# Optimization experiments

Hardware: AMD Instinct MI355X
Metric: run time of the kernel (lower is better)

## Reference

```python
import jax, jax.numpy as jnp
import numpy as np

B, L, C = 64, 64, 16          # batch, seq_len, chars per word
V, CV = 100000, 100           # word vocab, char vocab
EMB, CHD = 300, 64            # word emb dim, char emb dim
N_HIGHWAY, N_ATTN = 2, 2
D = EMB + 3 * 50              # highway_dim = 450


def setup_inputs() -> dict:
    ks = jax.random.split(jax.random.key(0), 16)
    word_emb = jax.random.normal(ks[6], (V, EMB), jnp.float32) * 0.01
    word_emb = word_emb.at[0].set(0.0)  # padding_idx row zeroed
    return {
        "q1": jax.random.randint(ks[0], (B, L), 0, V),
        "q2": jax.random.randint(ks[1], (B, L), 0, V),
        "q1_len": jax.random.randint(ks[2], (B,), 1, L + 1),
        "q2_len": jax.random.randint(ks[3], (B,), 1, L + 1),
        "q1_char": jax.random.randint(ks[4], (B, L, C), 0, CV),
        "q2_char": jax.random.randint(ks[5], (B, L, C), 0, CV),
        "word_emb": word_emb,
        "char_emb": jax.random.normal(ks[7], (CV, CHD), jnp.float32) * 0.1,
        "conv_w3": jax.random.normal(ks[8], (50, CHD, 3), jnp.float32) / np.sqrt(CHD * 3),
        "conv_b3": jnp.zeros((50,), jnp.float32),
        "conv_w4": jax.random.normal(ks[9], (50, CHD, 4), jnp.float32) / np.sqrt(CHD * 4),
        "conv_b4": jnp.zeros((50,), jnp.float32),
        "conv_w5": jax.random.normal(ks[10], (50, CHD, 5), jnp.float32) / np.sqrt(CHD * 5),
        "conv_b5": jnp.zeros((50,), jnp.float32),
        "hw_w": jax.random.normal(ks[11], (D, D), jnp.float32) / np.sqrt(D),
        "hw_b": jnp.zeros((D,), jnp.float32),
        "attn_w": jax.random.normal(ks[12], (N_ATTN, 3 * D), jnp.float32) / np.sqrt(3 * D),
        "attn_b": jnp.zeros((N_ATTN,), jnp.float32),
    }


def _char_features(qc, emb, convs):
    # qc: [B, T, C] int -> [B, T, 150]
    Bq, T, Cc = qc.shape
    e = emb[qc.reshape(-1, Cc)].transpose(0, 2, 1)  # [B*T, CHD, C]
    outs = []
    for w, b in convs:
        h = jax.lax.conv_general_dilated(e, w, (1,), 'VALID',
                                         dimension_numbers=('NCH', 'OIH', 'NCH'))
        h = jax.nn.relu(h + b[None, :, None])
        outs.append(jnp.max(h, axis=2))  # max over char positions
    return jnp.concatenate(outs, axis=-1).reshape(Bq, T, -1)


def _highway(x, w, b):
    # NB: original reuses the SAME linear for transform and gate (bug-faithful)
    y = x @ w.T + b
    g = jax.nn.sigmoid(y)
    return g * jax.nn.relu(y) + (1.0 - g) * x


def _self_attn(x, mask, w, b):
    # Exact decomposition of Linear(concat(x_i, x_j, x_i*x_j)) -> scalar:
    # score[b,i,j] = x_i.w1 + x_j.w2 + sum_d x_i x_j w3 + b
    d = x.shape[-1]
    w1, w2, w3 = w[:d], w[d:2 * d], w[2 * d:]
    scores = ((x @ w1)[:, :, None] + (x @ w2)[:, None, :]
              + jnp.einsum('bid,bjd->bij', x * w3, x) + b)
    # original masked_fill uses -1e-09 (not -1e9) -- reproduce faithfully
    logits = jnp.where(mask[:, None, :], scores, jnp.float32(-1e-9))
    attn = jax.nn.softmax(logits, axis=-1)
    return jnp.einsum('bij,bjd->bid', attn, x)


def _branch(q, q_char, q_len, word_emb, char_emb, convs, hw_w, hw_b, attn_w, attn_b):
    mask = jnp.arange(L)[None, :] < q_len[:, None]
    x = jnp.concatenate([word_emb[q], _char_features(q_char, char_emb, convs)], axis=-1)
    for _ in range(N_HIGHWAY):
        x = _highway(x, hw_w, hw_b)
    att = x
    for i in range(N_ATTN):
        att = _self_attn(x, mask, attn_w[i], attn_b[i])
        x = att + x
    return att


def reference(q1, q2, q1_len, q2_len, q1_char, q2_char, word_emb, char_emb,
              conv_w3, conv_b3, conv_w4, conv_b4, conv_w5, conv_b5,
              hw_w, hw_b, attn_w, attn_b):
    convs = [(conv_w3, conv_b3), (conv_w4, conv_b4), (conv_w5, conv_b5)]
    a1 = _branch(q1, q1_char, q1_len, word_emb, char_emb, convs, hw_w, hw_b, attn_w, attn_b)
    a2 = _branch(q2, q2_char, q2_len, word_emb, char_emb, convs, hw_w, hw_b, attn_w, attn_b)
    return (a1, a2)
```

## Files before the change

kernel.cpp:

```cpp
#include <hip/hip_runtime.h>
#include <math.h>

#define B   64
#define L   64
#define C   16
#define CHD 64
#define EMB 300
#define D   450
#define DP  480
#define NT  (B*L)
#define NBH 128

typedef short bf16x8 __attribute__((ext_vector_type(8)));
typedef float f32x4  __attribute__((ext_vector_type(4)));
typedef float f32x2  __attribute__((ext_vector_type(2)));
typedef unsigned short ushort_t;
typedef ushort_t us4 __attribute__((ext_vector_type(4)));

#define MFMA16 __builtin_amdgcn_mfma_f32_16x16x32_bf16

#define WPF_N (10 * 10 * 512)
#define WBF_N (32 * 15 * 512)
#define XFRAG 30720

#define XFS 456
#define XSS 488

__device__ inline float wave_sum(float v) {
#pragma unroll
    for (int o = 32; o; o >>= 1) v += __shfl_xor(v, o, 64);
    return v;
}
__device__ inline ushort_t f2b(float f) {
    union { float f; unsigned u; } c; c.f = f;
    unsigned r = c.u + 0x7FFFu + ((c.u >> 16) & 1u);
    return (ushort_t)(r >> 16);
}

__global__ __launch_bounds__(256) void prep_kernel(
    const float* __restrict__ W,
    const float* __restrict__ w3, const float* __restrict__ b3,
    const float* __restrict__ w4, const float* __restrict__ b4,
    const float* __restrict__ w5, const float* __restrict__ b5,
    const float* __restrict__ char_emb,
    ushort_t* __restrict__ Wb16F, ushort_t* __restrict__ WpadF,
    float* __restrict__ bias160, ushort_t* __restrict__ ceb16)
{
    int idx = blockIdx.x * 256 + threadIdx.x;
    if (idx < WBF_N) {
        const int e = idx & 7, l = (idx >> 3) & 63, t = idx >> 9;
        const int ks = t % 15, nt = t / 15;
        const int ln = l & 15, q = l >> 4;
        const int n = nt * 16 + ln, k = ks * 32 + q * 8 + e;
        float v = (n < D && k < D) ? W[(size_t)n * D + k] : 0.f;
        Wb16F[idx] = f2b(v);
        return;
    }
    idx -= WBF_N;
    if (idx < WPF_N) {
        const int e = idx & 7, l = (idx >> 3) & 63, t = idx >> 9;
        const int ks = t % 10, nt = t / 10;
        const int ln = l & 15, q = l >> 4;
        const int f = nt * 16 + ln;
        const int kd = ks * 32 + q * 8 + e;
        const int k = kd >> 6, d = kd & 63;
        float v = 0.f;
        if (f < 50)       { if (k < 3) v = w3[f * 192 + d * 3 + k]; }
        else if (f < 100) { if (k < 4) v = w4[(f - 50) * 256 + d * 4 + k]; }
        else if (f < 150) { v = w5[(f - 100) * 320 + d * 5 + k]; }
        WpadF[idx] = f2b(v);
        return;
    }
    idx -= WPF_N;
    if (idx < 160) {
        bias160[idx] = (idx < 50) ? b3[idx] : (idx < 100) ? b4[idx - 50]
                     : (idx < 150) ? b5[idx - 100] : 0.f;
    } else if (idx < 160 + 100 * 64) {
        int i = idx - 160;
        ceb16[i] = f2b(char_emb[i]);
    }
}

#define ESS 72
#define EST (20 * ESS)

__global__ __launch_bounds__(256) void embed_conv_kernel(
    const int* __restrict__ q1, const int* __restrict__ q2,
    const int* __restrict__ q1c, const int* __restrict__ q2c,
    const float* __restrict__ word_emb, const ushort_t* __restrict__ ceb16,
    const ushort_t* __restrict__ WpadF, const float* __restrict__ bias160,
    float* __restrict__ xout, ushort_t* __restrict__ xbF)
{
    __shared__ ushort_t es[8 * EST];
    __shared__ ushort_t Xt[8 * XSS];

    const int tid  = threadIdx.x;
    const int wv   = tid >> 6;
    const int lane = tid & 63;
    const int ln   = lane & 15, quad = lane >> 4;
    const int bx   = blockIdx.x;
    const int tokbase = ((bx & 7) * 128 + (bx >> 3)) * 8;

#pragma unroll
    for (int i = 0; i < 4; ++i) {
        int c = tid + i * 256;
        int row = c >> 3, part = c & 7;
        int tl = row >> 4, cr = row & 15;
        int gtok   = tokbase + tl;
        int branch = gtok >> 12;
        int tokl   = gtok & (NT - 1);
        int cid    = (branch ? q2c : q1c)[tokl * C + cr];
        *(bf16x8*)&es[tl * EST + cr * ESS + part * 8] =
            *(const bf16x8*)&ceb16[cid * 64 + part * 8];
    }
    {
        int tl = tid >> 5, rr = (tid >> 3) & 3, part = tid & 7;
        bf16x8 z = {0, 0, 0, 0, 0, 0, 0, 0};
        *(bf16x8*)&es[tl * EST + (16 + rr) * ESS + part * 8] = z;
    }

#pragma unroll 1
    for (int c = tid; c < 8 * 75; c += 256) {
        const int t  = c / 75, d4 = c - t * 75;
        const int tok    = tokbase + t;
        const int branch = tok >> 12;
        const int tokl   = tok & (NT - 1);
        const int w      = (branch ? q2 : q1)[tokl];
        const float4 v = *(const float4*)(word_emb + (size_t)w * EMB + d4 * 4);
        float* dst = xout + (size_t)tok * D + d4 * 4;
        *(f32x2*)dst       = (f32x2){v.x, v.y};
        *(f32x2*)(dst + 2) = (f32x2){v.z, v.w};
        us4 pk = { f2b(v.x), f2b(v.y), f2b(v.z), f2b(v.w) };
        *(us4*)&Xt[t * XSS + d4 * 4] = pk;
    }
    if (tid < 240) {
        const int t = tid / 30, k = tid - t * 30;
        Xt[t * XSS + D + k] = 0;
    }
    __syncthreads();

    const int t0 = wv * 2, t1 = t0 + 1;
    f32x4 acc[2][10];
#pragma unroll
    for (int t = 0; t < 2; ++t)
#pragma unroll
        for (int nt = 0; nt < 10; ++nt) acc[t][nt] = (f32x4){0.f, 0.f, 0.f, 0.f};

#pragma unroll 1
    for (int ks = 0; ks < 10; ++ks) {
        const int kk   = ks * 32 + quad * 8;
        const int arow = kk >> 6, aoff = kk & 63;
        bf16x8 a0 = *(const bf16x8*)&es[t0 * EST + (ln + arow) * ESS + aoff];
        bf16x8 a1 = *(const bf16x8*)&es[t1 * EST + (ln + arow) * ESS + aoff];
#pragma unroll
        for (int nt = 0; nt < 10; ++nt) {
            bf16x8 bf = *(const bf16x8*)&WpadF[(size_t)((nt * 10 + ks) << 9) + lane * 8];
            acc[0][nt] = MFMA16(a0, bf, acc[0][nt], 0, 0, 0);
            acc[1][nt] = MFMA16(a1, bf, acc[1][nt], 0, 0, 0);
        }
    }
    __syncthreads();

    float* smf = (float*)es;
#pragma unroll
    for (int t = 0; t < 2; ++t) {
        const int tloc = t0 + t;
#pragma unroll
        for (int nt = 0; nt < 10; ++nt) {
            const int f  = nt * 16 + ln;
            const int Pf = (f < 50) ? 14 : (f < 100) ? 13 : 12;
            float m = -1e30f;
#pragma unroll
            for (int r = 0; r < 4; ++r) {
                const int p = quad * 4 + r;
                if (p < Pf) m = fmaxf(m, acc[t][nt][r]);
            }
            m = fmaxf(m, __shfl_xor(m, 16, 64));
            m = fmaxf(m, __shfl_xor(m, 32, 64));
            if (quad == 0) smf[tloc * 160 + f] = fmaxf(0.f, m + bias160[f]);
        }
    }
    __syncthreads();
#pragma unroll 1
    for (int c = tid; c < 8 * 150; c += 256) {
        const int t = c / 150, f = c - t * 150;
        const float rv = smf[t * 160 + f];
        xout[(size_t)(tokbase + t) * D + EMB + f] = rv;
        Xt[t * XSS + EMB + f] = f2b(rv);
    }
    __syncthreads();

    {
        const int tile = tokbase >> 4, half = (tokbase >> 3) & 1;
#pragma unroll 1
        for (int c = tid; c < 480; c += 256) {
            const int ksl = c >> 5, s = c & 31;
            const int q = s >> 3, tl = s & 7;
            const int l = q * 16 + half * 8 + tl;
            bf16x8 v = *(const bf16x8*)&Xt[tl * XSS + ksl * 32 + q * 8];
            *(bf16x8*)&xbF[((size_t)(tile * 15 + ksl) * 64 + l) * 8] = v;
        }
    }
}

#define HLS 72

__global__ __launch_bounds__(256, 4) void highway_mfma_kernel(
    const ushort_t* __restrict__ xbFi, const float* __restrict__ xf32,
    const ushort_t* __restrict__ Wb16F, const float* __restrict__ bvec,
    float* __restrict__ out, ushort_t* __restrict__ xbFo)
{
    __shared__ ushort_t Xl[64 * HLS];

    const int bx = blockIdx.x;
    const int cx = bx & 7, rr = bx >> 3;
    const int my = cx * 16 + (rr & 15);
    const int mx = rr >> 4;

    const int tid  = threadIdx.x;
    const int wv   = tid >> 6;
    const int lane = tid & 63;
    const int wm = wv >> 1, wn = wv & 1;
    const int m0 = my * 64 + wm * 32;
    const int n0 = mx * 64 + wn * 32;
    const int lm = lane & 15, quad = lane >> 4;

    const int tA0 = my * 4 + wm * 2;
    const ushort_t* ax0 = xbFi + (size_t)(tA0 * 15) * 512 + lane * 8;
    const ushort_t* ax1 = ax0 + 15 * 512;
    const int ntg0 = mx * 4 + wn * 2;
    const ushort_t* bw0 = Wb16F + (size_t)(ntg0 * 15) * 512 + lane * 8;
    const ushort_t* bw1 = bw0 + 15 * 512;

    f32x4 acc[2][2];
#pragma unroll
    for (int i = 0; i < 2; ++i)
#pragma unroll
        for (int j = 0; j < 2; ++j) acc[i][j] = (f32x4){0.f, 0.f, 0.f, 0.f};

#pragma unroll 3
    for (int ks = 0; ks < 15; ++ks) {
        bf16x8 a0 = *(const bf16x8*)(ax0 + ks * 512);
        bf16x8 a1 = *(const bf16x8*)(ax1 + ks * 512);
        bf16x8 b0 = *(const bf16x8*)(bw0 + ks * 512);
        bf16x8 b1 = *(const bf16x8*)(bw1 + ks * 512);
        acc[0][0] = MFMA16(a0, b0, acc[0][0], 0, 0, 0);
        acc[0][1] = MFMA16(a0, b1, acc[0][1], 0, 0, 0);
        acc[1][0] = MFMA16(a1, b0, acc[1][0], 0, 0, 0);
        acc[1][1] = MFMA16(a1, b1, acc[1][1], 0, 0, 0);
    }

#pragma unroll
    for (int nt = 0; nt < 2; ++nt) {
        const int n  = n0 + nt * 16 + lm;
        const int nl = wn * 32 + nt * 16 + lm;
        const bool nval = (n < D);
        const float bv = nval ? bvec[n] : 0.f;
#pragma unroll
        for (int mt = 0; mt < 2; ++mt) {
#pragma unroll
            for (int r = 0; r < 4; ++r) {
                const int m  = m0 + mt * 16 + quad * 4 + r;
                const int ml = wm * 32 + mt * 16 + quad * 4 + r;
                float y = acc[mt][nt][r] + bv;
                float g = 1.f / (1.f + __expf(-y));
                float o = 0.f;
                if (nval) {
                    float xo = xf32[(size_t)m * D + n];
                    o = g * fmaxf(y, 0.f) + (1.f - g) * xo;
                    out[(size_t)m * D + n] = o;
                }
                Xl[ml * HLS + nl] = f2b(nval ? o : 0.f);
            }
        }
    }
    __syncthreads();

#pragma unroll 1
    for (int c = tid; c < 512; c += 256) {
        const int fi = c >> 6, l = c & 63;
        const int tl = fi >> 1, ksl = fi & 1;
        const int ksg = mx * 2 + ksl;
        if (ksg < 15) {
            const int lnp = l & 15, qp = l >> 4;
            bf16x8 v = *(const bf16x8*)&Xl[(tl * 16 + lnp) * HLS + ksl * 32 + qp * 8];
            *(bf16x8*)&xbFo[((size_t)((my * 4 + tl) * 15 + ksg) * 64 + l) * 8] = v;
        }
    }
}

__global__ __launch_bounds__(256) void highway2_prep_kernel(
    const ushort_t* __restrict__ xbFi, const float* __restrict__ xf32in,
    const ushort_t* __restrict__ Wb16F, const float* __restrict__ bvec,
    const float* __restrict__ attn_w,
    float* __restrict__ outf, ushort_t* __restrict__ xbFo,
    ushort_t* __restrict__ xw3F, ushort_t* __restrict__ xTF,
    float* __restrict__ s1g, float* __restrict__ s2g)
{
    __shared__ float    Xf[16 * XFS];
    __shared__ ushort_t Xs[16 * XSS];

    const int bx  = blockIdx.x;
    const int wid = (bx & 7) * 64 + (bx >> 3);
    const int bh  = wid >> 2, jq = wid & 3;
    const int tt  = wid;
    const int m0  = tt * 16;
    const int tid = threadIdx.x;
    const int wv  = tid >> 6;
    const int lane = tid & 63;
    const int ln = lane & 15, quad = lane >> 4;

    if (tid < 480) {
        const int t = tid / 30, k = tid - t * 30;
        Xs[t * XSS + D + k] = 0;
    }

    const ushort_t* ax = xbFi + (size_t)(tt * 15) * 512 + lane * 8;
    f32x4 acc[8];
#pragma unroll
    for (int t = 0; t < 8; ++t) acc[t] = (f32x4){0.f, 0.f, 0.f, 0.f};

#pragma unroll 1
    for (int ks = 0; ks < 15; ++ks) {
        bf16x8 a = *(const bf16x8*)(ax + ks * 512);
#pragma unroll
        for (int t = 0; t < 8; ++t) {
            const int nt = wv * 8 + t;
            if (nt < 30) {
                bf16x8 b = *(const bf16x8*)&Wb16F[(size_t)(nt * 15 + ks) * 512 + lane * 8];
                acc[t] = MFMA16(a, b, acc[t], 0, 0, 0);
            }
        }
    }

#pragma unroll
    for (int t = 0; t < 8; ++t) {
        const int nt = wv * 8 + t;
        if (nt >= 30) continue;
        const int n = nt * 16 + ln;
        const bool nval = (n < D);
        const float bv = nval ? bvec[n] : 0.f;
#pragma unroll
        for (int reg = 0; reg < 4; ++reg) {
            const int i = quad * 4 + reg;
            float y = acc[t][reg] + bv;
            float g = 1.f / (1.f + __expf(-y));
            if (nval) {
                float xo = xf32in[(size_t)(m0 + i) * D + n];
                float o = g * fmaxf(y, 0.f) + (1.f - g) * xo;
                outf[(size_t)(m0 + i) * D + n] = o;
                Xf[i * XFS + n] = o;
                Xs[i * XSS + n] = f2b(o);
            }
        }
    }
    __syncthreads();

    const float* wb = attn_w;
    const float* w3 = wb + 2 * D;

#pragma unroll 1
    for (int rr = 0; rr < 4; ++rr) {
        const int j = wv * 4 + rr;
        float a1 = 0.f, a2 = 0.f;
#pragma unroll
        for (int t = 0; t < 8; ++t) {
            const int k = lane + t * 64;
            if (k < D) {
                float xv = Xf[j * XFS + k];
                a1 = fmaf(xv, wb[k], a1);
                a2 = fmaf(xv, wb[D + k], a2);
            }
        }
        a1 = wave_sum(a1);
        a2 = wave_sum(a2);
        if (lane == 0) { s1g[m0 + j] = a1; s2g[m0 + j] = a2; }
    }

#pragma unroll 1
    for (int c = tid; c < 960; c += 256) {
        const int ks = c >> 6, l = c & 63;
        const int lnp = l & 15, qp = l >> 4;
        bf16x8 v = *(const bf16x8*)&Xs[lnp * XSS + ks * 32 + qp * 8];
        *(bf16x8*)&xbFo[((size_t)(tt * 15 + ks) * 64 + l) * 8] = v;
        bf16x8 pv;
#pragma unroll
        for (int e = 0; e < 8; ++e) {
            const int k = ks * 32 + qp * 8 + e;
            const float x = (k < D) ? Xf[lnp * XFS + k] : 0.f;
            pv[e] = (short)f2b((k < D) ? x * w3[k] : 0.f);
        }
        *(bf16x8*)&xw3F[(size_t)bh * XFRAG + ((jq * 15 + ks) * 64 + l) * 8] = pv;
    }

    {
        const int half = jq >> 1, q0 = (jq & 1) * 2;
#pragma unroll 1
        for (int c = tid; c < 960; c += 256) {
            const int dt = c >> 5, s = c & 31;
            const int qp = q0 + (s >> 4), lnp = s & 15;
            const int d  = dt * 16 + lnp;
            const int jb = (qp & 1) * 8;
            bf16x8 v;
#pragma unroll
            for (int e = 0; e < 8; ++e) v[e] = (short)Xs[(jb + e) * XSS + d];
            *(bf16x8*)&xTF[(size_t)bh * XFRAG + ((dt * 2 + half) * 64 + qp * 16 + lnp) * 8] = v;
        }
    }
}

#define ALS 72

__global__ __launch_bounds__(256) void attn_core_prep_kernel(
    const float* __restrict__ xf32,
    const ushort_t* __restrict__ xF, const ushort_t* __restrict__ xw3F,
    const ushort_t* __restrict__ xTF,
    const float* __restrict__ s1g, const float* __restrict__ s2g,
    const int* __restrict__ q1_len, const int* __restrict__ q2_len,
    const float* __restrict__ attn_b, const float* __restrict__ attn_w,
    ushort_t* __restrict__ xbFo,
    ushort_t* __restrict__ xw3Fo, ushort_t* __restrict__ xTFo,
    float* __restrict__ s1o, float* __restrict__ s2o)
{
    __shared__ float    sc[16][68];
    __shared__ ushort_t Al[16 * ALS];
    __shared__ float    Af[16 * XFS];
    __shared__ ushort_t At[16 * XSS];

    const int bx  = blockIdx.x;
    const int wid = (bx & 7) * 64 + (bx >> 3);
    const int bh  = wid >> 2, iq = wid & 3;
    const int branch = bh >> 6, b = bh & 63;
    const int tid  = threadIdx.x;
    const int wv   = tid >> 6;
    const int lane = tid & 63;
    const int ln   = lane & 15, quad = lane >> 4;
    const int i0   = iq * 16;
    const int m0   = bh * 64 + i0;

    if (tid < 480) {
        const int t = tid / 30, k = tid - t * 30;
        At[t * XSS + D + k] = 0;
    }

    const ushort_t* xa = xF   + (size_t)bh * XFRAG + (iq * 15 * 64 + lane) * 8;
    const ushort_t* xb = xw3F + (size_t)bh * XFRAG + (wv * 15 * 64 + lane) * 8;

    f32x4 qa0 = (f32x4){0.f, 0.f, 0.f, 0.f};
    f32x4 qa1 = (f32x4){0.f, 0.f, 0.f, 0.f};
#pragma unroll
    for (int ks = 0; ks < 14; ks += 2) {
        bf16x8 a0 = *(const bf16x8*)(xa + ks * 512);
        bf16x8 b0 = *(const bf16x8*)(xb + ks * 512);
        bf16x8 a1 = *(const bf16x8*)(xa + ks * 512 + 512);
        bf16x8 b1 = *(const bf16x8*)(xb + ks * 512 + 512);
        qa0 = MFMA16(a0, b0, qa0, 0, 0, 0);
        qa1 = MFMA16(a1, b1, qa1, 0, 0, 0);
    }
    {
        bf16x8 a  = *(const bf16x8*)(xa + 14 * 512);
        bf16x8 bq = *(const bf16x8*)(xb + 14 * 512);
        qa0 = MFMA16(a, bq, qa0, 0, 0, 0);
    }
    f32x4 qacc = qa0 + qa1;

    const int   len  = (branch ? q2_len : q1_len)[b];
    const float bias = attn_b[0];
    const int   j    = wv * 16 + ln;
    const float s2v  = s2g[bh * 64 + j];
#pragma unroll
    for (int reg = 0; reg < 4; ++reg) {
        const int i = i0 + quad * 4 + reg;
        float v = qacc[reg] + s1g[bh * 64 + i] + s2v + bias;
        if (j >= len) v = -1e-9f;
        sc[quad * 4 + reg][j] = v;
    }
    __syncthreads();

#pragma unroll
    for (int rr = 0; rr < 4; ++rr) {
        const int r = wv * 4 + rr;
        float v = sc[r][lane];
        float m = v;
#pragma unroll
        for (int o = 32; o; o >>= 1) m = fmaxf(m, __shfl_xor(m, o, 64));
        float ev = __expf(v - m);
        float sm = ev;
#pragma unroll
        for (int o = 32; o; o >>= 1) sm += __shfl_xor(sm, o, 64);
        Al[r * ALS + lane] = f2b(ev * (1.f / sm));
    }
    __syncthreads();

    const ushort_t* xTb = xTF + (size_t)bh * XFRAG + lane * 8;
    bf16x8 af0 = *(const bf16x8*)&Al[ln * ALS + quad * 8];
    bf16x8 af1 = *(const bf16x8*)&Al[ln * ALS + quad * 8 + 32];

#pragma unroll 2
    for (int dt = wv; dt < 30; dt += 4) {
        bf16x8 b0 = *(const bf16x8*)(xTb + dt * 1024);
        bf16x8 b1 = *(const bf16x8*)(xTb + dt * 1024 + 512);
        f32x4 acc = (f32x4){0.f, 0.f, 0.f, 0.f};
        acc = MFMA16(af0, b0, acc, 0, 0, 0);
        acc = MFMA16(af1, b1, acc, 0, 0, 0);

        const int d = dt * 16 + ln;
        if (d < D) {
#pragma unroll
            for (int reg = 0; reg < 4; ++reg) {
                const int il = quad * 4 + reg;
                float v = acc[reg] + xf32[(size_t)(m0 + il) * D + d];
                Af[il * XFS + d] = v;
                At[il * XSS + d] = f2b(v);
            }
        }
    }
    __syncthreads();

    const float* wb1 = attn_w + 3 * D;
    const float* w31 = wb1 + 2 * D;

#pragma unroll 1
    for (int rr = 0; rr < 4; ++rr) {
        const int jj = wv * 4 + rr;
        float a1 = 0.f, a2 = 0.f;
#pragma unroll
        for (int t = 0; t < 8; ++t) {
            const int k = lane + t * 64;
            if (k < D) {
                float xv = Af[jj * XFS + k];
                a1 = fmaf(xv, wb1[k], a1);
                a2 = fmaf(xv, wb1[D + k], a2);
            }
        }
        a1 = wave_sum(a1);
        a2 = wave_sum(a2);
        if (lane == 0) { s1o[m0 + jj] = a1; s2o[m0 + jj] = a2; }
    }

#pragma unroll 1
    for (int c = tid; c < 960; c += 256) {
        const int ks = c >> 6, l = c & 63;
        const int lnp = l & 15, qp = l >> 4;
        bf16x8 v = *(const bf16x8*)&At[lnp * XSS + ks * 32 + qp * 8];
        *(bf16x8*)&xbFo[((size_t)((bh * 4 + iq) * 15 + ks) * 64 + l) * 8] = v;
        bf16x8 pv;
#pragma unroll
        for (int e = 0; e < 8; ++e) {
            const int k = ks * 32 + qp * 8 + e;
            const float x = (k < D) ? Af[lnp * XFS + k] : 0.f;
            pv[e] = (short)f2b((k < D) ? x * w31[k] : 0.f);
        }
        *(bf16x8*)&xw3Fo[(size_t)bh * XFRAG + ((iq * 15 + ks) * 64 + l) * 8] = pv;
    }

    {
        const int half = iq >> 1, q0 = (iq & 1) * 2;
#pragma unroll 1
        for (int c = tid; c < 960; c += 256) {
            const int dt = c >> 5, s = c & 31;
            const int qp = q0 + (s >> 4), lnp = s & 15;
            const int d  = dt * 16 + lnp;
            const int jb = (qp & 1) * 8;
            bf16x8 v;
#pragma unroll
            for (int e = 0; e < 8; ++e) v[e] = (short)At[(jb + e) * XSS + d];
            *(bf16x8*)&xTFo[(size_t)bh * XFRAG + ((dt * 2 + half) * 64 + qp * 16 + lnp) * 8] = v;
        }
    }
}

__global__ __launch_bounds__(256) void attn_core_final_kernel(
    const ushort_t* __restrict__ xF, const ushort_t* __restrict__ xw3F,
    const ushort_t* __restrict__ xTF,
    const float* __restrict__ s1g, const float* __restrict__ s2g,
    const int* __restrict__ q1_len, const int* __restrict__ q2_len,
    const float* __restrict__ attn_b,
    float* __restrict__ outf)
{
    __shared__ float    sc[16][68];
    __shared__ ushort_t Al[16 * ALS];

    const int bx  = blockIdx.x;
    const int wid = (bx & 7) * 64 + (bx >> 3);
    const int bh  = wid >> 2, iq = wid & 3;
    const int branch = bh >> 6, b = bh & 63;
    const int tid  = threadIdx.x;
    const int wv   = tid >> 6;
    const int lane = tid & 63;
    const int ln   = lane & 15, quad = lane >> 4;
    const int i0   = iq * 16;

    const ushort_t* xa = xF   + (size_t)bh * XFRAG + (iq * 15 * 64 + lane) * 8;
    const ushort_t* xb = xw3F + (size_t)bh * XFRAG + (wv * 15 * 64 + lane) * 8;

    f32x4 qa0 = (f32x4){0.f, 0.f, 0.f, 0.f};
    f32x4 qa1 = (f32x4){0.f, 0.f, 0.f, 0.f};
#pragma unroll
    for (int ks = 0; ks < 14; ks += 2) {
        bf16x8 a0 = *(const bf16x8*)(xa + ks * 512);
        bf16x8 b0 = *(const bf16x8*)(xb + ks * 512);
        bf16x8 a1 = *(const bf16x8*)(xa + ks * 512 + 512);
        bf16x8 b1 = *(const bf16x8*)(xb + ks * 512 + 512);
        qa0 = MFMA16(a0, b0, qa0, 0, 0, 0);
        qa1 = MFMA16(a1, b1, qa1, 0, 0, 0);
    }
    {
        bf16x8 a  = *(const bf16x8*)(xa + 14 * 512);
        bf16x8 bq = *(const bf16x8*)(xb + 14 * 512);
        qa0 = MFMA16(a, bq, qa0, 0, 0, 0);
    }
    f32x4 qacc = qa0 + qa1;

    const int   len  = (branch ? q2_len : q1_len)[b];
    const float bias = attn_b[1];
    const int   j    = wv * 16 + ln;
    const float s2v  = s2g[bh * 64 + j];
#pragma unroll
    for (int reg = 0; reg < 4; ++reg) {
        const int i = i0 + quad * 4 + reg;
        float v = qacc[reg] + s1g[bh * 64 + i] + s2v + bias;
        if (j >= len) v = -1e-9f;
        sc[quad * 4 + reg][j] = v;
    }
    __syncthreads();

#pragma unroll
    for (int rr = 0; rr < 4; ++rr) {
        const int r = wv * 4 + rr;
        float v = sc[r][lane];
        float m = v;
#pragma unroll
        for (int o = 32; o; o >>= 1) m = fmaxf(m, __shfl_xor(m, o, 64));
        float ev = __expf(v - m);
        float sm = ev;
#pragma unroll
        for (int o = 32; o; o >>= 1) sm += __shfl_xor(sm, o, 64);
        Al[r * ALS + lane] = f2b(ev * (1.f / sm));
    }
    __syncthreads();

    const ushort_t* xTb = xTF + (size_t)bh * XFRAG + lane * 8;
    bf16x8 af0 = *(const bf16x8*)&Al[ln * ALS + quad * 8];
    bf16x8 af1 = *(const bf16x8*)&Al[ln * ALS + quad * 8 + 32];

#pragma unroll 2
    for (int dt = wv; dt < 30; dt += 4) {
        bf16x8 b0 = *(const bf16x8*)(xTb + dt * 1024);
        bf16x8 b1 = *(const bf16x8*)(xTb + dt * 1024 + 512);
        f32x4 acc = (f32x4){0.f, 0.f, 0.f, 0.f};
        acc = MFMA16(af0, b0, acc, 0, 0, 0);
        acc = MFMA16(af1, b1, acc, 0, 0, 0);

        const int d = dt * 16 + ln;
        if (d < D) {
#pragma unroll
            for (int reg = 0; reg < 4; ++reg) {
                const int i = i0 + quad * 4 + reg;
                outf[((size_t)bh * 64 + i) * D + d] = acc[reg];
            }
        }
    }
}

extern "C" void kernel_launch(void* const* d_in, const int* in_sizes, int n_in,
                              void* d_out, int out_size, void* d_ws, size_t ws_size,
                              hipStream_t stream) {
    const int*   q1       = (const int*)  d_in[0];
    const int*   q2       = (const int*)  d_in[1];
    const int*   q1_len   = (const int*)  d_in[2];
    const int*   q2_len   = (const int*)  d_in[3];
    const int*   q1c      = (const int*)  d_in[4];
    const int*   q2c      = (const int*)  d_in[5];
    const float* word_emb = (const float*)d_in[6];
    const float* char_emb = (const float*)d_in[7];
    const float* w3       = (const float*)d_in[8];
    const float* b3       = (const float*)d_in[9];
    const float* w4       = (const float*)d_in[10];
    const float* b4       = (const float*)d_in[11];
    const float* w5       = (const float*)d_in[12];
    const float* b5       = (const float*)d_in[13];
    const float* hw_w     = (const float*)d_in[14];
    const float* hw_b     = (const float*)d_in[15];
    const float* attn_w   = (const float*)d_in[16];
    const float* attn_b   = (const float*)d_in[17];
    float* out = (float*)d_out;

    float*    buf0    = (float*)d_ws;
    float*    buf1    = buf0 + (size_t)2 * NT * D;
    float*    bias160 = buf1 + (size_t)2 * NT * D;
    ushort_t* xbFa    = (ushort_t*)(bias160 + 160);
    ushort_t* xbFb    = xbFa + (size_t)2 * NT * DP;
    ushort_t* Wb16F   = xbFb + (size_t)2 * NT * DP;
    ushort_t* WpadF   = Wb16F + (size_t)WBF_N;
    ushort_t* ceb16   = WpadF + (size_t)WPF_N;
    ushort_t* xw3Fa   = ceb16 + (size_t)100 * 64;
    ushort_t* xTFa    = xw3Fa + (size_t)NBH * XFRAG;
    ushort_t* xw3Fb   = xTFa  + (size_t)NBH * XFRAG;
    ushort_t* xTFb    = xw3Fb + (size_t)NBH * XFRAG;
    float*    s1a     = (float*)(xTFb + (size_t)NBH * XFRAG);
    float*    s2a     = s1a + (size_t)2 * NT;
    float*    s1b     = s2a + (size_t)2 * NT;
    float*    s2b     = s1b + (size_t)2 * NT;

    prep_kernel<<<(WBF_N + WPF_N + 160 + 100 * 64 + 255) / 256, 256, 0, stream>>>(
        hw_w, w3, b3, w4, b4, w5, b5, char_emb, Wb16F, WpadF, bias160, ceb16);
    embed_conv_kernel<<<1024, 256, 0, stream>>>(q1, q2, q1c, q2c, word_emb, ceb16,
                                                WpadF, bias160, buf0, xbFa);

    highway_mfma_kernel<<<1024, 256, 0, stream>>>(xbFa, buf0, Wb16F, hw_b, buf1, xbFb);

    highway2_prep_kernel<<<512, 256, 0, stream>>>(
        xbFb, buf1, Wb16F, hw_b, attn_w, buf0, xbFa, xw3Fa, xTFa, s1a, s2a);

    attn_core_prep_kernel<<<512, 256, 0, stream>>>(
        buf0, xbFa, xw3Fa, xTFa, s1a, s2a, q1_len, q2_len, attn_b, attn_w,
        xbFb, xw3Fb, xTFb, s1b, s2b);

    attn_core_final_kernel<<<512, 256, 0, stream>>>(
        xbFb, xw3Fb, xTFb, s1b, s2b, q1_len, q2_len, attn_b, out);
}
```

Baseline: 324.0 us.

## Double threads per block in highway2 and attention kernels, split-K score GEMM

Grows highway2_prep, attn_core_prep and attn_core_final from 256 to 512 threads with the same 512-block grid. Each wave now handles half the N-tiles, rows and d-tiles. In the attention kernels the score GEMM's K loop is split across two wave groups, with the partial sums reduced through a new shared Qp buffer and an extra barrier. The bf16 shared copies (Xs/At) are dropped; bf16 values are converted from the fp32 tile when fragments are written out, which cuts LDS use but adds conversion work.

```diff
diff --git a/kernel.cpp b/kernel.cpp
--- a/kernel.cpp
+++ b/kernel.cpp
@@ -289,7 +289,7 @@
     }
 }
 
-__global__ __launch_bounds__(256) void highway2_prep_kernel(
+__global__ __launch_bounds__(512, 4) void highway2_prep_kernel(
     const ushort_t* __restrict__ xbFi, const float* __restrict__ xf32in,
     const ushort_t* __restrict__ Wb16F, const float* __restrict__ bvec,
     const float* __restrict__ attn_w,
@@ -297,8 +297,7 @@
     ushort_t* __restrict__ xw3F, ushort_t* __restrict__ xTF,
     float* __restrict__ s1g, float* __restrict__ s2g)
 {
-    __shared__ float    Xf[16 * XFS];
-    __shared__ ushort_t Xs[16 * XSS];
+    __shared__ float Xf[16 * XFS];
 
     const int bx  = blockIdx.x;
     const int wid = (bx & 7) * 64 + (bx >> 3);
@@ -310,22 +309,17 @@
     const int lane = tid & 63;
     const int ln = lane & 15, quad = lane >> 4;
 
-    if (tid < 480) {
-        const int t = tid / 30, k = tid - t * 30;
-        Xs[t * XSS + D + k] = 0;
-    }
-
     const ushort_t* ax = xbFi + (size_t)(tt * 15) * 512 + lane * 8;
-    f32x4 acc[8];
-#pragma unroll
-    for (int t = 0; t < 8; ++t) acc[t] = (f32x4){0.f, 0.f, 0.f, 0.f};
+    f32x4 acc[4];
+#pragma unroll
+    for (int t = 0; t < 4; ++t) acc[t] = (f32x4){0.f, 0.f, 0.f, 0.f};
 
 #pragma unroll 1
     for (int ks = 0; ks < 15; ++ks) {
         bf16x8 a = *(const bf16x8*)(ax + ks * 512);
 #pragma unroll
-        for (int t = 0; t < 8; ++t) {
-            const int nt = wv * 8 + t;
+        for (int t = 0; t < 4; ++t) {
+            const int nt = wv * 4 + t;
             if (nt < 30) {
                 bf16x8 b = *(const bf16x8*)&Wb16F[(size_t)(nt * 15 + ks) * 512 + lane * 8];
                 acc[t] = MFMA16(a, b, acc[t], 0, 0, 0);
@@ -334,8 +328,8 @@
     }
 
 #pragma unroll
-    for (int t = 0; t < 8; ++t) {
-        const int nt = wv * 8 + t;
+    for (int t = 0; t < 4; ++t) {
+        const int nt = wv * 4 + t;
         if (nt >= 30) continue;
         const int n = nt * 16 + ln;
         const bool nval = (n < D);
@@ -350,7 +344,6 @@
                 float o = g * fmaxf(y, 0.f) + (1.f - g) * xo;
                 outf[(size_t)(m0 + i) * D + n] = o;
                 Xf[i * XFS + n] = o;
-                Xs[i * XSS + n] = f2b(o);
             }
         }
     }
@@ -360,8 +353,8 @@
     const float* w3 = wb + 2 * D;
 
 #pragma unroll 1
-    for (int rr = 0; rr < 4; ++rr) {
-        const int j = wv * 4 + rr;
+    for (int rr = 0; rr < 2; ++rr) {
+        const int j = wv * 2 + rr;
         float a1 = 0.f, a2 = 0.f;
 #pragma unroll
         for (int t = 0; t < 8; ++t) {
@@ -378,32 +371,33 @@
     }
 
 #pragma unroll 1
-    for (int c = tid; c < 960; c += 256) {
+    for (int c = tid; c < 960; c += 512) {
         const int ks = c >> 6, l = c & 63;
         const int lnp = l & 15, qp = l >> 4;
-        bf16x8 v = *(const bf16x8*)&Xs[lnp * XSS + ks * 32 + qp * 8];
-        *(bf16x8*)&xbFo[((size_t)(tt * 15 + ks) * 64 + l) * 8] = v;
-        bf16x8 pv;
+        bf16x8 v, pv;
 #pragma unroll
         for (int e = 0; e < 8; ++e) {
             const int k = ks * 32 + qp * 8 + e;
             const float x = (k < D) ? Xf[lnp * XFS + k] : 0.f;
+            v[e]  = (short)((k < D) ? f2b(x) : 0);
             pv[e] = (short)f2b((k < D) ? x * w3[k] : 0.f);
         }
+        *(bf16x8*)&xbFo[((size_t)(tt * 15 + ks) * 64 + l) * 8] = v;
         *(bf16x8*)&xw3F[(size_t)bh * XFRAG + ((jq * 15 + ks) * 64 + l) * 8] = pv;
     }
 
     {
         const int half = jq >> 1, q0 = (jq & 1) * 2;
 #pragma unroll 1
-        for (int c = tid; c < 960; c += 256) {
+        for (int c = tid; c < 960; c += 512) {
             const int dt = c >> 5, s = c & 31;
             const int qp = q0 + (s >> 4), lnp = s & 15;
             const int d  = dt * 16 + lnp;
             const int jb = (qp & 1) * 8;
             bf16x8 v;
 #pragma unroll
-            for (int e = 0; e < 8; ++e) v[e] = (short)Xs[(jb + e) * XSS + d];
+            for (int e = 0; e < 8; ++e)
+                v[e] = (short)((d < D) ? f2b(Xf[(jb + e) * XFS + d]) : 0);
             *(bf16x8*)&xTF[(size_t)bh * XFRAG + ((dt * 2 + half) * 64 + qp * 16 + lnp) * 8] = v;
         }
     }
@@ -411,7 +405,7 @@
 
 #define ALS 72
 
-__global__ __launch_bounds__(256) void attn_core_prep_kernel(
+__global__ __launch_bounds__(512, 4) void attn_core_prep_kernel(
     const float* __restrict__ xf32,
     const ushort_t* __restrict__ xF, const ushort_t* __restrict__ xw3F,
     const ushort_t* __restrict__ xTF,
@@ -424,8 +418,8 @@
 {
     __shared__ float    sc[16][68];
     __shared__ ushort_t Al[16 * ALS];
+    __shared__ float    Qp[4 * 256];
     __shared__ float    Af[16 * XFS];
-    __shared__ ushort_t At[16 * XSS];
 
     const int bx  = blockIdx.x;
     const int wid = (bx & 7) * 64 + (bx >> 3);
@@ -437,49 +431,50 @@
     const int ln   = lane & 15, quad = lane >> 4;
     const int i0   = iq * 16;
     const int m0   = bh * 64 + i0;
-
-    if (tid < 480) {
-        const int t = tid / 30, k = tid - t * 30;
-        At[t * XSS + D + k] = 0;
-    }
+    const int jt   = wv & 3, hks = wv >> 2;
 
     const ushort_t* xa = xF   + (size_t)bh * XFRAG + (iq * 15 * 64 + lane) * 8;
-    const ushort_t* xb = xw3F + (size_t)bh * XFRAG + (wv * 15 * 64 + lane) * 8;
-
-    f32x4 qa0 = (f32x4){0.f, 0.f, 0.f, 0.f};
-    f32x4 qa1 = (f32x4){0.f, 0.f, 0.f, 0.f};
-#pragma unroll
-    for (int ks = 0; ks < 14; ks += 2) {
-        bf16x8 a0 = *(const bf16x8*)(xa + ks * 512);
-        bf16x8 b0 = *(const bf16x8*)(xb + ks * 512);
-        bf16x8 a1 = *(const bf16x8*)(xa + ks * 512 + 512);
-        bf16x8 b1 = *(const bf16x8*)(xb + ks * 512 + 512);
-        qa0 = MFMA16(a0, b0, qa0, 0, 0, 0);
-        qa1 = MFMA16(a1, b1, qa1, 0, 0, 0);
-    }
-    {
-        bf16x8 a  = *(const bf16x8*)(xa + 14 * 512);
-        bf16x8 bq = *(const bf16x8*)(xb + 14 * 512);
-        qa0 = MFMA16(a, bq, qa0, 0, 0, 0);
-    }
-    f32x4 qacc = qa0 + qa1;
+    const ushort_t* xb = xw3F + (size_t)bh * XFRAG + (jt * 15 * 64 + lane) * 8;
+
+    f32x4 qa = (f32x4){0.f, 0.f, 0.f, 0.f};
+    if (hks == 0) {
+#pragma unroll
+        for (int ks = 0; ks < 15; ks += 2) {
+            bf16x8 a  = *(const bf16x8*)(xa + ks * 512);
+            bf16x8 bq = *(const bf16x8*)(xb + ks * 512);
+            qa = MFMA16(a, bq, qa, 0, 0, 0);
+        }
+    } else {
+#pragma unroll
+        for (int ks = 1; ks < 15; ks += 2) {
+            bf16x8 a  = *(const bf16x8*)(xa + ks * 512);
+            bf16x8 bq = *(const bf16x8*)(xb + ks * 512);
+            qa = MFMA16(a, bq, qa, 0, 0, 0);
+        }
+        *(f32x4*)&Qp[jt * 256 + lane * 4] = qa;
+    }
+    __syncthreads();
 
     const int   len  = (branch ? q2_len : q1_len)[b];
-    const float bias = attn_b[0];
-    const int   j    = wv * 16 + ln;
-    const float s2v  = s2g[bh * 64 + j];
-#pragma unroll
-    for (int reg = 0; reg < 4; ++reg) {
-        const int i = i0 + quad * 4 + reg;
-        float v = qacc[reg] + s1g[bh * 64 + i] + s2v + bias;
-        if (j >= len) v = -1e-9f;
-        sc[quad * 4 + reg][j] = v;
-    }
-    __syncthreads();
-
-#pragma unroll
-    for (int rr = 0; rr < 4; ++rr) {
-        const int r = wv * 4 + rr;
+    if (hks == 0) {
+        f32x4 qo = *(const f32x4*)&Qp[jt * 256 + lane * 4];
+        f32x4 qacc = qa + qo;
+        const float bias = attn_b[0];
+        const int   j    = jt * 16 + ln;
+        const float s2v  = s2g[bh * 64 + j];
+#pragma unroll
+        for (int reg = 0; reg < 4; ++reg) {
+            const int i = i0 + quad * 4 + reg;
+            float v = qacc[reg] + s1g[bh * 64 + i] + s2v + bias;
+            if (j >= len) v = -1e-9f;
+            sc[quad * 4 + reg][j] = v;
+        }
+    }
+    __syncthreads();
+
+#pragma unroll
+    for (int rr = 0; rr < 2; ++rr) {
+        const int r = wv * 2 + rr;
         float v = sc[r][lane];
         float m = v;
 #pragma unroll
@@ -497,7 +492,7 @@
     bf16x8 af1 = *(const bf16x8*)&Al[ln * ALS + quad * 8 + 32];
 
 #pragma unroll 2
-    for (int dt = wv; dt < 30; dt += 4) {
+    for (int dt = wv; dt < 30; dt += 8) {
         bf16x8 b0 = *(const bf16x8*)(xTb + dt * 1024);
         bf16x8 b1 = *(const bf16x8*)(xTb + dt * 1024 + 512);
         f32x4 acc = (f32x4){0.f, 0.f, 0.f, 0.f};
@@ -511,7 +506,6 @@
                 const int il = quad * 4 + reg;
                 float v = acc[reg] + xf32[(size_t)(m0 + il) * D + d];
                 Af[il * XFS + d] = v;
-                At[il * XSS + d] = f2b(v);
             }
         }
     }
@@ -521,8 +515,8 @@
     const float* w31 = wb1 + 2 * D;
 
 #pragma unroll 1
-    for (int rr = 0; rr < 4; ++rr) {
-        const int jj = wv * 4 + rr;
+    for (int rr = 0; rr < 2; ++rr) {
+        const int jj = wv * 2 + rr;
         float a1 = 0.f, a2 = 0.f;
 #pragma unroll
         for (int t = 0; t < 8; ++t) {
@@ -539,38 +533,39 @@
     }
 
 #pragma unroll 1
-    for (int c = tid; c < 960; c += 256) {
+    for (int c = tid; c < 960; c += 512) {
         const int ks = c >> 6, l = c & 63;
         const int lnp = l & 15, qp = l >> 4;
-        bf16x8 v = *(const bf16x8*)&At[lnp * XSS + ks * 32 + qp * 8];
-        *(bf16x8*)&xbFo[((size_t)((bh * 4 + iq) * 15 + ks) * 64 + l) * 8] = v;
-        bf16x8 pv;
+        bf16x8 v, pv;
 #pragma unroll
         for (int e = 0; e < 8; ++e) {
             const int k = ks * 32 + qp * 8 + e;
             const float x = (k < D) ? Af[lnp * XFS + k] : 0.f;
+            v[e]  = (short)((k < D) ? f2b(x) : 0);
             pv[e] = (short)f2b((k < D) ? x * w31[k] : 0.f);
         }
+        *(bf16x8*)&xbFo[((size_t)((bh * 4 + iq) * 15 + ks) * 64 + l) * 8] = v;
         *(bf16x8*)&xw3Fo[(size_t)bh * XFRAG + ((iq * 15 + ks) * 64 + l) * 8] = pv;
     }
 
     {
         const int half = iq >> 1, q0 = (iq & 1) * 2;
 #pragma unroll 1
-        for (int c = tid; c < 960; c += 256) {
+        for (int c = tid; c < 960; c += 512) {
             const int dt = c >> 5, s = c & 31;
             const int qp = q0 + (s >> 4), lnp = s & 15;
             const int d  = dt * 16 + lnp;
             const int jb = (qp & 1) * 8;
             bf16x8 v;
 #pragma unroll
-            for (int e = 0; e < 8; ++e) v[e] = (short)At[(jb + e) * XSS + d];
+            for (int e = 0; e < 8; ++e)
+                v[e] = (short)((d < D) ? f2b(Af[(jb + e) * XFS + d]) : 0);
             *(bf16x8*)&xTFo[(size_t)bh * XFRAG + ((dt * 2 + half) * 64 + qp * 16 + lnp) * 8] = v;
         }
     }
 }
 
-__global__ __launch_bounds__(256) void attn_core_final_kernel(
+__global__ __launch_bounds__(512, 4) void attn_core_final_kernel(
     const ushort_t* __restrict__ xF, const ushort_t* __restrict__ xw3F,
     const ushort_t* __restrict__ xTF,
     const float* __restrict__ s1g, const float* __restrict__ s2g,
@@ -580,6 +575,7 @@
 {
     __shared__ float    sc[16][68];
     __shared__ ushort_t Al[16 * ALS];
+    __shared__ float    Qp[4 * 256];
 
     const int bx  = blockIdx.x;
     const int wid = (bx & 7) * 64 + (bx >> 3);
@@ -590,44 +586,50 @@
     const int lane = tid & 63;
     const int ln   = lane & 15, quad = lane >> 4;
     const int i0   = iq * 16;
+    const int jt   = wv & 3, hks = wv >> 2;
 
     const ushort_t* xa = xF   + (size_t)bh * XFRAG + (iq * 15 * 64 + lane) * 8;
-    const ushort_t* xb = xw3F + (size_t)bh * XFRAG + (wv * 15 * 64 + lane) * 8;
-
-    f32x4 qa0 = (f32x4){0.f, 0.f, 0.f, 0.f};
-    f32x4 qa1 = (f32x4){0.f, 0.f, 0.f, 0.f};
-#pragma unroll
-    for (int ks = 0; ks < 14; ks += 2) {
-        bf16x8 a0 = *(const bf16x8*)(xa + ks * 512);
-        bf16x8 b0 = *(const bf16x8*)(xb + ks * 512);
-        bf16x8 a1 = *(const bf16x8*)(xa + ks * 512 + 512);
-        bf16x8 b1 = *(const bf16x8*)(xb + ks * 512 + 512);
-        qa0 = MFMA16(a0, b0, qa0, 0, 0, 0);
-        qa1 = MFMA16(a1, b1, qa1, 0, 0, 0);
-    }
-    {
-        bf16x8 a  = *(const bf16x8*)(xa + 14 * 512);
-        bf16x8 bq = *(const bf16x8*)(xb + 14 * 512);
-        qa0 = MFMA16(a, bq, qa0, 0, 0, 0);
-    }
-    f32x4 qacc = qa0 + qa1;
-
-    const int   len  = (branch ? q2_len : q1_len)[b];
-    const float bias = attn_b[1];
-    const int   j    = wv * 16 + ln;
-    const float s2v  = s2g[bh * 64 + j];
-#pragma unroll
-    for (int reg = 0; reg < 4; ++reg) {
-        const int i = i0 + quad * 4 + reg;
-        float v = qacc[reg] + s1g[bh * 64 + i] + s2v + bias;
-        if (j >= len) v = -1e-9f;
-        sc[quad * 4 + reg][j] = v;
-    }
-    __syncthreads();
-
-#pragma unroll
-    for (int rr = 0; rr < 4; ++rr) {
-        const int r = wv * 4 + rr;
+    const ushort_t* xb = xw3F + (size_t)bh * XFRAG + (jt * 15 * 64 + lane) * 8;
+
+    f32x4 qa = (f32x4){0.f, 0.f, 0.f, 0.f};
+    if (hks == 0) {
+#pragma unroll
+        for (int ks = 0; ks < 15; ks += 2) {
+            bf16x8 a  = *(const bf16x8*)(xa + ks * 512);
+            bf16x8 bq = *(const bf16x8*)(xb + ks * 512);
+            qa = MFMA16(a, bq, qa, 0, 0, 0);
+        }
+    } else {
+#pragma unroll
+        for (int ks = 1; ks < 15; ks += 2) {
+            bf16x8 a  = *(const bf16x8*)(xa + ks * 512);
+            bf16x8 bq = *(const bf16x8*)(xb + ks * 512);
+            qa = MFMA16(a, bq, qa, 0, 0, 0);
+        }
+        *(f32x4*)&Qp[jt * 256 + lane * 4] = qa;
+    }
+    __syncthreads();
+
+    const int len = (branch ? q2_len : q1_len)[b];
+    if (hks == 0) {
+        f32x4 qo = *(const f32x4*)&Qp[jt * 256 + lane * 4];
+        f32x4 qacc = qa + qo;
+        const float bias = attn_b[1];
+        const int   j    = jt * 16 + ln;
+        const float s2v  = s2g[bh * 64 + j];
+#pragma unroll
+        for (int reg = 0; reg < 4; ++reg) {
+            const int i = i0 + quad * 4 + reg;
+            float v = qacc[reg] + s1g[bh * 64 + i] + s2v + bias;
+            if (j >= len) v = -1e-9f;
+            sc[quad * 4 + reg][j] = v;
+        }
+    }
+    __syncthreads();
+
+#pragma unroll
+    for (int rr = 0; rr < 2; ++rr) {
+        const int r = wv * 2 + rr;
         float v = sc[r][lane];
         float m = v;
 #pragma unroll
@@ -645,7 +647,7 @@
     bf16x8 af1 = *(const bf16x8*)&Al[ln * ALS + quad * 8 + 32];
 
 #pragma unroll 2
-    for (int dt = wv; dt < 30; dt += 4) {
+    for (int dt = wv; dt < 30; dt += 8) {
         bf16x8 b0 = *(const bf16x8*)(xTb + dt * 1024);
         bf16x8 b1 = *(const bf16x8*)(xTb + dt * 1024 + 512);
         f32x4 acc = (f32x4){0.f, 0.f, 0.f, 0.f};
@@ -710,13 +712,13 @@
 
     highway_mfma_kernel<<<1024, 256, 0, stream>>>(xbFa, buf0, Wb16F, hw_b, buf1, xbFb);
 
-    highway2_prep_kernel<<<512, 256, 0, stream>>>(
+    highway2_prep_kernel<<<512, 512, 0, stream>>>(
         xbFb, buf1, Wb16F, hw_b, attn_w, buf0, xbFa, xw3Fa, xTFa, s1a, s2a);
 
-    attn_core_prep_kernel<<<512, 256, 0, stream>>>(
+    attn_core_prep_kernel<<<512, 512, 0, stream>>>(
         buf0, xbFa, xw3Fa, xTFa, s1a, s2a, q1_len, q2_len, attn_b, attn_w,
         xbFb, xw3Fb, xTFb, s1b, s2b);
 
-    attn_core_final_kernel<<<512, 256, 0, stream>>>(
+    attn_core_final_kernel<<<512, 512, 0, stream>>>(
         xbFb, xw3Fb, xTFb, s1b, s2b, q1_len, q2_len, attn_b, out);
 }
```

After: 306.0 us. 1.06x faster.
